# Optimization experiments

Measured on AMD Instinct MI355X. Metric: run time of the kernel, lower is better.

Reference implementation:

```python
import jax, jax.numpy as jnp
import numpy as np

B, T, DIM = 4, 1024, 2048
H, KVH = 16, 4
HD = DIM // H          # 128
G = H // KVH           # GQA group size = 4


def setup_inputs() -> dict:
    key = jax.random.key(0)
    ks = jax.random.split(key, 4)
    s = 1.0 / np.sqrt(DIM)
    x = jax.random.normal(ks[0], (B, T, DIM), jnp.float32)
    Wq = jax.random.normal(ks[1], (DIM, DIM), jnp.float32) * s
    Wkv = jax.random.normal(ks[2], (DIM, 2 * KVH * HD), jnp.float32) * s
    Wo = jax.random.normal(ks[3], (DIM, DIM), jnp.float32) * s
    # RoPE tables (theta=10000, half-split / rotate-half convention)
    inv_freq = 1.0 / (10000.0 ** (np.arange(0, HD, 2, dtype=np.float64) / HD))
    freqs = np.outer(np.arange(T, dtype=np.float64), inv_freq)  # [T, HD/2]
    cos = jnp.asarray(np.cos(freqs), jnp.float32)
    sin = jnp.asarray(np.sin(freqs), jnp.float32)
    return {"x": x, "Wq": Wq, "Wkv": Wkv, "Wo": Wo, "cos": cos, "sin": sin}


def _rope(u, cos, sin):
    # u: [B,T,heads,HD]; cos/sin: [T, HD/2]
    u1, u2 = jnp.split(u, 2, axis=-1)
    c = cos[None, :, None, :]
    s = sin[None, :, None, :]
    return jnp.concatenate([u1 * c - u2 * s, u1 * s + u2 * c], axis=-1)


def reference(x, Wq, Wkv, Wo, cos, sin):
    Bs, Ts, C = x.shape
    q = (x @ Wq).reshape(Bs, Ts, H, HD)
    kv = (x @ Wkv).reshape(Bs, Ts, 2, KVH, HD)
    k, v = kv[:, :, 0], kv[:, :, 1]
    q = _rope(q, cos, sin)
    k = _rope(k, cos, sin)
    # GQA without materializing repeated K/V: fold group dim into q
    qg = q.reshape(Bs, Ts, KVH, G, HD)
    scores = jnp.einsum('bqhgd,bkhd->bhgqk', qg, k) / np.float32(np.sqrt(HD))
    causal = jnp.tril(jnp.ones((Ts, Ts), bool))
    neg = jnp.finfo(scores.dtype).min
    scores = jnp.where(causal, scores, neg)
    att = jax.nn.softmax(scores, axis=-1)
    out = jnp.einsum('bhgqk,bkhd->bqhgd', att, v).reshape(Bs, Ts, C)
    return out @ Wo
```

## Files before the change

kernel.cpp:

```cpp
#include <hip/hip_runtime.h>

typedef unsigned short u16;
typedef unsigned int u32;
typedef __bf16 bf16x8 __attribute__((ext_vector_type(8)));
typedef float f32x4 __attribute__((ext_vector_type(4)));

#define BB   4
#define TT   1024
#define CDIM 2048
#define NH   16
#define NKV  4
#define HDIM 128

__device__ __forceinline__ float b2f(u16 u) {
    union { u32 i; float f; } x; x.i = ((u32)u) << 16; return x.f;
}
__device__ __forceinline__ u16 f2b(float f) {
    union { float f; u32 i; } x; x.f = f;
    u32 r = (x.i + 0x7fffu + ((x.i >> 16) & 1u)) >> 16;
    return (u16)r;
}
__device__ __forceinline__ void async16(const void* g, void* l) {
    __builtin_amdgcn_global_load_lds((const __attribute__((address_space(1))) void*)g,
                                     (__attribute__((address_space(3))) void*)l, 16, 0, 0);
}
template<int N> __device__ __forceinline__ void waitvm() {
    static_assert(N == 0 || N == 3 || N == 4 || N == 6 || N == 7, "unsupported vmcnt");
    if constexpr (N == 0)      asm volatile("s_waitcnt vmcnt(0)" ::: "memory");
    else if constexpr (N == 3) asm volatile("s_waitcnt vmcnt(3)" ::: "memory");
    else if constexpr (N == 4) asm volatile("s_waitcnt vmcnt(4)" ::: "memory");
    else if constexpr (N == 6) asm volatile("s_waitcnt vmcnt(6)" ::: "memory");
    else                       asm volatile("s_waitcnt vmcnt(7)" ::: "memory");
}

__device__ __forceinline__ bool wave_is_f32(const u16* xp) {
    u16 v = xp[(threadIdx.x & 63) * 2];
    int e = (v >> 7) & 0xFF;
    bool bad = (v != 0) && (e < 90 || e > 160);
    return __popcll(__ballot(bad)) > 16;
}

__global__ __launch_bounds__(256) void pre_k(const void* __restrict__ x,
                                             const void* __restrict__ Wq,
                                             const void* __restrict__ Wkv,
                                             const void* __restrict__ Wo,
                                             u16* __restrict__ xb,
                                             u16* __restrict__ csb,
                                             u16* __restrict__ snb,
                                             u16* __restrict__ WqkvT,
                                             u16* __restrict__ WoT,
                                             const void* __restrict__ cs,
                                             const void* __restrict__ sn) {
    const bool f32m = wave_is_f32((const u16*)x);
    int bid = blockIdx.x;
    if (bid < 8320) {
        const void* src; u16* dst; int i;
        if (bid < 8192)      { src = x;  dst = xb;  i = bid * 256 + threadIdx.x; }
        else if (bid < 8256) { src = cs; dst = csb; i = (bid - 8192) * 256 + threadIdx.x; }
        else                 { src = sn; dst = snb; i = (bid - 8256) * 256 + threadIdx.x; }
        union { u16 u[4]; ushort4 v; } o;
        if (f32m) {
            float4 f = ((const float4*)src)[i];
            o.u[0] = f2b(f.x); o.u[1] = f2b(f.y); o.u[2] = f2b(f.z); o.u[3] = f2b(f.w);
        } else {
            o.v = ((const ushort4*)src)[i];
        }
        ((ushort4*)dst)[i] = o.v;
        return;
    }
    __shared__ alignas(16) u16 tile[64 * 65];
    int t = bid - 8320;
    const void* W; u16* WT; int rows, cols, bx, by;
    if (t < 1024)      { W = Wq;  WT = WqkvT;                    rows = 2048; cols = 2048; bx = t & 31;  by = t >> 5; }
    else if (t < 1536) { int l = t - 1024; W = Wkv; WT = WqkvT + (long)2048 * 2048; rows = 2048; cols = 1024; bx = l & 15; by = l >> 4; }
    else               { int l = t - 1536; W = Wo;  WT = WoT;  rows = 2048; cols = 2048; bx = l & 31;   by = l >> 5; }
    const int r0 = by * 64, c0 = bx * 64;
#pragma unroll
    for (int i = 0; i < 16; i++) {
        int c = threadIdx.x + i * 256;
        int rr = c >> 6, cc = c & 63;
        long idx = (long)(r0 + rr) * cols + c0 + cc;
        tile[rr * 65 + cc] = f32m ? f2b(((const float*)W)[idx]) : ((const u16*)W)[idx];
    }
    __syncthreads();
#pragma unroll
    for (int i = 0; i < 16; i++) {
        int c = threadIdx.x + i * 256;
        int rr = c >> 6, cc = c & 63;
        WT[(long)(c0 + rr) * rows + r0 + cc] = tile[cc * 65 + rr];
    }
}

template<int BM, int BN>
__global__ __launch_bounds__(512, 2) void gemm_t(const u16* __restrict__ A,
                                                 const u16* __restrict__ Bt,
                                                 void* __restrict__ C,
                                                 int N, int Kd,
                                                 const u16* __restrict__ xprobe) {
    constexpr int MF  = BM / 32;
    constexpr int NF  = BN / 64;
    constexpr int MF0 = MF / 2, MF1 = MF - MF0;
    constexpr int NF0 = (NF + 1) / 2, NF1 = NF - NF0;
    constexpr int NAU = BM / 64;
    constexpr int NBU = BN / 64;

    __shared__ alignas(16) u16 As[2][BM * 64];
    __shared__ alignas(16) u16 Bs[2][BN * 64];

    const bool f32m = (xprobe != nullptr) && wave_is_f32(xprobe);
    const int tid = threadIdx.x;
    const int w = tid >> 6, lane = tid & 63;
    const int wm = w >> 2, wn = w & 3;
    const int l16 = lane & 15, quad = lane >> 4;
    const long arow0 = (long)blockIdx.y * BM;
    const long brow0 = (long)blockIdx.x * BN;
    const int NT = Kd >> 6;

    const int srow = tid >> 3, scp = tid & 7;
    const long gst = (long)srow * Kd + ((scp ^ (srow & 7)) << 3);
    const int cst = tid << 3;

    const u16* Ab = A + arow0 * Kd;
    const u16* Bb = Bt + brow0 * Kd;

    auto stageA = [&](int buf, int t) {
#pragma unroll
        for (int u = 0; u < NAU; u++)
            async16(Ab + (long)u * 64 * Kd + t * 64 + gst, &As[buf][u * 4096 + cst]);
    };
    auto stageB = [&](int buf, int t) {
#pragma unroll
        for (int u = 0; u < NBU; u++)
            async16(Bb + (long)u * 64 * Kd + t * 64 + gst, &Bs[buf][u * 4096 + cst]);
    };

    const int R0a = wm * (BM / 2) + l16, sA = R0a & 7;
    const int R0b = wn * (BN / 4) + l16, sB = R0b & 7;
    int aoff[2], boff[2];
    aoff[0] = R0a * 64 + ((quad ^ sA) << 3);
    aoff[1] = R0a * 64 + (((4 + quad) ^ sA) << 3);
    boff[0] = R0b * 64 + ((quad ^ sB) << 3);
    boff[1] = R0b * 64 + (((4 + quad) ^ sB) << 3);

    f32x4 acc[MF][NF];
#pragma unroll
    for (int i = 0; i < MF; i++)
#pragma unroll
        for (int j = 0; j < NF; j++) acc[i][j] = {0.f, 0.f, 0.f, 0.f};

    stageB(0, 0); stageA(0, 0); stageB(1, 1); stageA(1, 1);
    waitvm<NAU + NBU>();
    __builtin_amdgcn_s_barrier();

#pragma unroll 1
    for (int t = 0; t < NT; ++t) {
        const int cur = t & 1;
        const u16* pA = &As[cur][0];
        const u16* pB = &Bs[cur][0];
        bf16x8 afLo[MF0][2], afHi[MF1][2], bfA[NF0][2], bfB[NF1][2];

#pragma unroll
        for (int ks = 0; ks < 2; ks++) {
#pragma unroll
            for (int mt = 0; mt < MF0; mt++)
                afLo[mt][ks] = *(const bf16x8*)&pA[aoff[ks] + mt * 1024];
#pragma unroll
            for (int nt = 0; nt < NF0; nt++)
                bfA[nt][ks] = *(const bf16x8*)&pB[boff[ks] + nt * 1024];
#pragma unroll
            for (int nt = 0; nt < NF1; nt++)
                bfB[nt][ks] = *(const bf16x8*)&pB[boff[ks] + (NF0 + nt) * 1024];
        }
        asm volatile("s_waitcnt lgkmcnt(0)" ::: "memory");
        __builtin_amdgcn_sched_barrier(0);
        __builtin_amdgcn_s_setprio(1);
#pragma unroll
        for (int ks = 0; ks < 2; ks++)
#pragma unroll
            for (int mt = 0; mt < MF0; mt++) {
#pragma unroll
                for (int nt = 0; nt < NF0; nt++)
                    acc[mt][nt] = __builtin_amdgcn_mfma_f32_16x16x32_bf16(
                        afLo[mt][ks], bfA[nt][ks], acc[mt][nt], 0, 0, 0);
#pragma unroll
                for (int nt = 0; nt < NF1; nt++)
                    acc[mt][NF0 + nt] = __builtin_amdgcn_mfma_f32_16x16x32_bf16(
                        afLo[mt][ks], bfB[nt][ks], acc[mt][NF0 + nt], 0, 0, 0);
            }
        __builtin_amdgcn_s_setprio(0);

#pragma unroll
        for (int ks = 0; ks < 2; ks++)
#pragma unroll
            for (int mt = 0; mt < MF1; mt++)
                afHi[mt][ks] = *(const bf16x8*)&pA[aoff[ks] + (MF0 + mt) * 1024];
        __builtin_amdgcn_s_barrier();
        if (t + 2 < NT) stageB(cur, t + 2);
        asm volatile("s_waitcnt lgkmcnt(0)" ::: "memory");
        __builtin_amdgcn_sched_barrier(0);
        __builtin_amdgcn_s_setprio(1);
#pragma unroll
        for (int ks = 0; ks < 2; ks++)
#pragma unroll
            for (int mt = 0; mt < MF1; mt++) {
#pragma unroll
                for (int nt = 0; nt < NF1; nt++)
                    acc[MF0 + mt][NF0 + nt] = __builtin_amdgcn_mfma_f32_16x16x32_bf16(
                        afHi[mt][ks], bfB[nt][ks], acc[MF0 + mt][NF0 + nt], 0, 0, 0);
#pragma unroll
                for (int nt = 0; nt < NF0; nt++)
                    acc[MF0 + mt][nt] = __builtin_amdgcn_mfma_f32_16x16x32_bf16(
                        afHi[mt][ks], bfA[nt][ks], acc[MF0 + mt][nt], 0, 0, 0);
            }
        __builtin_amdgcn_s_setprio(0);

        if (t + 1 < NT) {
            if (t + 2 < NT) waitvm<NBU>();
            else            waitvm<0>();
            __builtin_amdgcn_s_barrier();
            if (t + 2 < NT) stageA(cur, t + 2);
        }
    }

#pragma unroll
    for (int mt = 0; mt < MF; mt++) {
#pragma unroll
        for (int nt = 0; nt < NF; nt++) {
            long col = brow0 + wn * (BN / 4) + nt * 16 + l16;
#pragma unroll
            for (int r = 0; r < 4; r++) {
                long row = arow0 + wm * (BM / 2) + mt * 16 + quad * 4 + r;
                if (f32m) ((float*)C)[row * N + col] = acc[mt][nt][r];
                else      ((u16*)C)[row * N + col] = f2b(acc[mt][nt][r]);
            }
        }
    }
}

__global__ __launch_bounds__(256) void prep_k(const u16* __restrict__ QKVraw,
                                              const u16* __restrict__ cs,
                                              const u16* __restrict__ sn,
                                              u16* __restrict__ Qr,
                                              u16* __restrict__ Kr,
                                              u16* __restrict__ Vt) {
    int bid = blockIdx.x;
    if (bid < 16384) {
        int idx = bid * 256 + threadIdx.x;
        int d = idx & 63;
        int t = (idx >> 6) & (TT - 1);
        int bh = idx >> 16;
        long src = ((long)((bh >> 4) * TT + t)) * 3072 + (bh & 15) * HDIM;
        float u1 = b2f(QKVraw[src + d]), u2 = b2f(QKVraw[src + d + 64]);
        float c = b2f(cs[t * 64 + d]), s = b2f(sn[t * 64 + d]);
        long dst = ((long)bh * TT + t) * HDIM;
        Qr[dst + d] = f2b(u1 * c - u2 * s);
        Qr[dst + d + 64] = f2b(u1 * s + u2 * c);
    } else if (bid < 20480) {
        int idx = (bid - 16384) * 256 + threadIdx.x;
        int d = idx & 63;
        int t = (idx >> 6) & (TT - 1);
        int bk = idx >> 16;
        long src = ((long)((bk >> 2) * TT + t)) * 3072 + 2048 + (bk & 3) * HDIM;
        float u1 = b2f(QKVraw[src + d]), u2 = b2f(QKVraw[src + d + 64]);
        float c = b2f(cs[t * 64 + d]), s = b2f(sn[t * 64 + d]);
        long dst = ((long)bk * TT + t) * HDIM;
        Kr[dst + d] = f2b(u1 * c - u2 * s);
        Kr[dst + d + 64] = f2b(u1 * s + u2 * c);
    } else {
        int idx = (bid - 20480) * 256 + threadIdx.x;
        int t = idx & (TT - 1);
        int d = (idx >> 10) & (HDIM - 1);
        int bk = idx >> 17;
        Vt[idx] = QKVraw[((long)(bk >> 2) * TT + t) * 3072 + 2560 + (bk & 3) * HDIM + d];
    }
}

__global__ __launch_bounds__(256) void attn_kernel(const u16* __restrict__ Q,
                                                   const u16* __restrict__ Kr,
                                                   const u16* __restrict__ Vt,
                                                   u16* __restrict__ O) {
    __shared__ alignas(16) u16 Ks[2][64 * 128];
    __shared__ alignas(16) u16 Vts[2][128 * 64];
    __shared__ alignas(16) u16 Ps[64 * 88];

    const int tid = threadIdx.x, w = tid >> 6, lane = tid & 63;
    const int l16 = lane & 15, quad = lane >> 4;
    const float scale2 = 0.08838834764831845f * 1.4426950408889634f;

#pragma unroll 1
    for (int it = 0; it < 2; it++) {
        const int j = it ? (1023 - (int)blockIdx.x) : (int)blockIdx.x;
        const int qt = 15 - (j >> 6);
        const int bh = j & 63;
        const int b = bh >> 4, h = bh & 15;
        const int kvh = h >> 2;
        const long qrow0 = (long)bh * TT + qt * 64;
        const long krow0 = (long)(b * NKV + kvh) * TT;
        const long vbase = ((long)(b * NKV + kvh) * HDIM) * TT;

        __syncthreads();

#pragma unroll
        for (int i = 0; i < 4; i++) {
            int slot0 = (w * 4 + i) * 64;
            int slot = slot0 + lane;
            int row = slot >> 4, cp = slot & 15;
            int cg = (cp & 8) | ((cp ^ row) & 7);
            async16(Q + (qrow0 + row) * HDIM + cg * 8, &Ks[0][slot0 * 8]);
        }
        asm volatile("s_waitcnt vmcnt(0)" ::: "memory");
        bf16x8 qf[4];
        {
            const int Rq = w * 16 + l16;
#pragma unroll
            for (int ds = 0; ds < 4; ds++) {
                int c = ds * 4 + quad;
                qf[ds] = *(const bf16x8*)&Ks[0][Rq * 128 + ((c & 8) | ((c ^ Rq) & 7)) * 8];
            }
        }
        asm volatile("s_waitcnt lgkmcnt(0)" ::: "memory");

#pragma unroll
        for (int i = 0; i < 4; i++) {
            int slot0 = (w * 4 + i) * 64;
            int slot = slot0 + lane;
            int row = slot >> 4, cp = slot & 15;
            int cg = (cp & 8) | ((cp ^ row) & 7);
            async16(Kr + (krow0 + row) * HDIM + cg * 8, &Ks[0][slot0 * 8]);
        }
#pragma unroll
        for (int i = 0; i < 4; i++) {
            int slot0 = (w * 4 + i) * 64;
            int slot = slot0 + lane;
            int row = slot >> 3, cp = slot & 7;
            int cg = cp ^ (row & 7);
            async16(Vt + vbase + (long)row * TT + cg * 8, &Vts[0][slot0 * 8]);
        }
        if (qt >= 1) {
#pragma unroll
            for (int i = 0; i < 4; i++) {
                int slot0 = (w * 4 + i) * 64;
                int slot = slot0 + lane;
                int row = slot >> 4, cp = slot & 15;
                int cg = (cp & 8) | ((cp ^ row) & 7);
                async16(Kr + (krow0 + 64 + row) * HDIM + cg * 8, &Ks[1][slot0 * 8]);
            }
#pragma unroll
            for (int i = 0; i < 4; i++) {
                int slot0 = (w * 4 + i) * 64;
                int slot = slot0 + lane;
                int row = slot >> 3, cp = slot & 7;
                int cg = cp ^ (row & 7);
                async16(Vt + vbase + (long)row * TT + 64 + cg * 8, &Vts[1][slot0 * 8]);
            }
            asm volatile("s_waitcnt vmcnt(8)" ::: "memory");
        } else {
            asm volatile("s_waitcnt vmcnt(0)" ::: "memory");
        }
        asm volatile("s_barrier" ::: "memory");

        f32x4 o[8];
#pragma unroll
        for (int i = 0; i < 8; i++) o[i] = {0.f, 0.f, 0.f, 0.f};
        float m_i = -1.0e30f, l_i = 0.f;
        const int qg = qt * 64 + w * 16 + l16;

#pragma unroll 1
        for (int kt = 0; kt <= qt; kt++) {
            const int cur = kt & 1;
            const u16* ksb = Ks[cur];
            const u16* vsb = Vts[cur];

            f32x4 s[4];
#pragma unroll
            for (int nt = 0; nt < 4; nt++) s[nt] = {0.f, 0.f, 0.f, 0.f};
#pragma unroll
            for (int ds = 0; ds < 4; ds++) {
                int c = ds * 4 + quad;
#pragma unroll
                for (int nt = 0; nt < 4; nt++) {
                    int Rk = nt * 16 + l16;
                    bf16x8 ak = *(const bf16x8*)&ksb[Rk * 128 + ((c & 8) | ((c ^ Rk) & 7)) * 8];
                    s[nt] = __builtin_amdgcn_mfma_f32_16x16x32_bf16(ak, qf[ds], s[nt], 0, 0, 0);
                }
            }

            float p[4][4];
            float mx = -1.0e30f;
            if (kt == qt) {
#pragma unroll
                for (int nt = 0; nt < 4; nt++)
#pragma unroll
                    for (int r = 0; r < 4; r++) {
                        int kcol = kt * 64 + nt * 16 + quad * 4 + r;
                        float v = (kcol <= qg) ? (float)s[nt][r] * scale2 : -1.0e30f;
                        p[nt][r] = v;
                        mx = fmaxf(mx, v);
                    }
            } else {
#pragma unroll
                for (int nt = 0; nt < 4; nt++)
#pragma unroll
                    for (int r = 0; r < 4; r++) {
                        float v = (float)s[nt][r] * scale2;
                        p[nt][r] = v;
                        mx = fmaxf(mx, v);
                    }
            }
            mx = fmaxf(mx, __shfl_xor(mx, 16));
            mx = fmaxf(mx, __shfl_xor(mx, 32));
            float mnew = fmaxf(m_i, mx);
            float alpha = exp2f(m_i - mnew);
            float rs = 0.f;
#pragma unroll
            for (int nt = 0; nt < 4; nt++)
#pragma unroll
                for (int r = 0; r < 4; r++) {
                    float e = exp2f(p[nt][r] - mnew);
                    p[nt][r] = e;
                    rs += e;
                }
            rs += __shfl_xor(rs, 16);
            rs += __shfl_xor(rs, 32);
            l_i = l_i * alpha + rs;

            u32* Psw = (u32*)Ps;
            int pb = (w * 16 + l16) * 44 + quad * 2;
#pragma unroll
            for (int nt = 0; nt < 4; nt++) {
                u32 lo = (u32)f2b(p[nt][0]) | ((u32)f2b(p[nt][1]) << 16);
                u32 hi = (u32)f2b(p[nt][2]) | ((u32)f2b(p[nt][3]) << 16);
                Psw[pb + nt * 8]     = lo;
                Psw[pb + nt * 8 + 1] = hi;
            }
            if (__ballot(mnew != m_i) != 0ULL) {
#pragma unroll
                for (int n8 = 0; n8 < 8; n8++)
#pragma unroll
                    for (int r = 0; r < 4; r++) o[n8][r] *= alpha;
            }
            m_i = mnew;

            asm volatile("s_waitcnt lgkmcnt(0)" ::: "memory");

#pragma unroll
            for (int ks = 0; ks < 2; ks++) {
                bf16x8 bp = *(const bf16x8*)&Ps[(w * 16 + l16) * 88 + ks * 32 + quad * 8];
#pragma unroll
                for (int n8 = 0; n8 < 8; n8++) {
                    int Rv = n8 * 16 + l16;
                    int c = ks * 4 + quad;
                    bf16x8 av = *(const bf16x8*)&vsb[Rv * 64 + (c ^ (Rv & 7)) * 8];
                    o[n8] = __builtin_amdgcn_mfma_f32_16x16x32_bf16(av, bp, o[n8], 0, 0, 0);
                }
            }

            if (kt == qt) break;

            asm volatile("s_waitcnt lgkmcnt(0)" ::: "memory");
            asm volatile("s_barrier" ::: "memory");
            if (kt + 2 <= qt) {
                const int nk = kt + 2;
#pragma unroll
                for (int i = 0; i < 4; i++) {
                    int slot0 = (w * 4 + i) * 64;
                    int slot = slot0 + lane;
                    int row = slot >> 4, cp = slot & 15;
                    int cg = (cp & 8) | ((cp ^ row) & 7);
                    async16(Kr + (krow0 + nk * 64 + row) * HDIM + cg * 8, &Ks[cur][slot0 * 8]);
                }
#pragma unroll
                for (int i = 0; i < 4; i++) {
                    int slot0 = (w * 4 + i) * 64;
                    int slot = slot0 + lane;
                    int row = slot >> 3, cp = slot & 7;
                    int cg = cp ^ (row & 7);
                    async16(Vt + vbase + (long)row * TT + nk * 64 + cg * 8, &Vts[cur][slot0 * 8]);
                }
                asm volatile("s_waitcnt vmcnt(8)" ::: "memory");
            } else {
                asm volatile("s_waitcnt vmcnt(0)" ::: "memory");
            }
            asm volatile("s_barrier" ::: "memory");
        }

        float inv = 1.0f / l_i;
        long obase = ((long)(b * TT + qg)) * CDIM + h * HDIM;
#pragma unroll
        for (int n8 = 0; n8 < 8; n8++) {
            ushort4 st;
            st.x = f2b(o[n8][0] * inv);
            st.y = f2b(o[n8][1] * inv);
            st.z = f2b(o[n8][2] * inv);
            st.w = f2b(o[n8][3] * inv);
            *(ushort4*)&O[obase + n8 * 16 + quad * 4] = st;
        }
    }
}

extern "C" void kernel_launch(void* const* d_in, const int* in_sizes, int n_in,
                              void* d_out, int out_size, void* d_ws, size_t ws_size,
                              hipStream_t stream) {
    const void* x   = d_in[0];
    const void* Wq  = d_in[1];
    const void* Wkv = d_in[2];
    const void* Wo  = d_in[3];
    const void* cs  = d_in[4];
    const void* sn  = d_in[5];

    char* ws = (char*)d_ws;
    const size_t NEED = 105119748;
    if (ws_size < NEED) return;

    u16* WqkvT = (u16*)(ws + 0);
    u16* WoT   = (u16*)(ws + 12582912);
    u16* QKVraw= (u16*)(ws + 20971520);
    u16* Qr    = (u16*)(ws + 46137344);
    u16* Kr    = (u16*)(ws + 62914560);
    u16* Vt    = (u16*)(ws + 67108864);
    u16* ATT   = (u16*)(ws + 71303168);
    u16* xb    = (u16*)(ws + 88080384);
    u16* csb   = (u16*)(ws + 104857600);
    u16* snb   = (u16*)(ws + 104988672);

    pre_k<<<10880, 256, 0, stream>>>(x, Wq, Wkv, Wo, xb, csb, snb, WqkvT, WoT, cs, sn);

    gemm_t<256, 192><<<dim3(16, 16), 512, 0, stream>>>(xb, WqkvT, QKVraw, 3072, 2048, nullptr);

    prep_k<<<28672, 256, 0, stream>>>(QKVraw, csb, snb, Qr, Kr, Vt);

    attn_kernel<<<512, 256, 0, stream>>>(Qr, Kr, Vt, ATT);

    gemm_t<128, 256><<<dim3(8, 32), 512, 0, stream>>>(ATT, WoT, d_out, 2048, 2048, (const u16*)x);
}
```

Before: 302.5 us.

## Split GEMM mainloop into four MFMA phases with interleaved half-tile async staging

Restructures the double-buffered bf16 GEMM mainloop into four compute phases, each preceded by LDS fragment loads, a barrier and an async global-to-LDS stage of half of the next tile's A or B rows. The prologue now preloads only half of the next B tile, and the rest of the next-tile loads are spread across the iteration. The goal is to interleave memory traffic with MFMA work more finely and shorten the exposed wait per iteration. In exchange it adds more barriers per iteration and a full vmcnt(0) wait, which could add stalls.

```diff
diff --git a/kernel.cpp b/kernel.cpp
--- a/kernel.cpp
+++ b/kernel.cpp
@@ -25,12 +25,16 @@
                                      (__attribute__((address_space(3))) void*)l, 16, 0, 0);
 }
 template<int N> __device__ __forceinline__ void waitvm() {
-    static_assert(N == 0 || N == 3 || N == 4 || N == 6 || N == 7, "unsupported vmcnt");
+    static_assert(N >= 0 && N <= 8, "unsupported vmcnt");
     if constexpr (N == 0)      asm volatile("s_waitcnt vmcnt(0)" ::: "memory");
+    else if constexpr (N == 1) asm volatile("s_waitcnt vmcnt(1)" ::: "memory");
+    else if constexpr (N == 2) asm volatile("s_waitcnt vmcnt(2)" ::: "memory");
     else if constexpr (N == 3) asm volatile("s_waitcnt vmcnt(3)" ::: "memory");
     else if constexpr (N == 4) asm volatile("s_waitcnt vmcnt(4)" ::: "memory");
+    else if constexpr (N == 5) asm volatile("s_waitcnt vmcnt(5)" ::: "memory");
     else if constexpr (N == 6) asm volatile("s_waitcnt vmcnt(6)" ::: "memory");
-    else                       asm volatile("s_waitcnt vmcnt(7)" ::: "memory");
+    else if constexpr (N == 7) asm volatile("s_waitcnt vmcnt(7)" ::: "memory");
+    else                       asm volatile("s_waitcnt vmcnt(8)" ::: "memory");
 }
 
 __device__ __forceinline__ bool wave_is_f32(const u16* xp) {
@@ -103,6 +107,8 @@
     constexpr int NF0 = (NF + 1) / 2, NF1 = NF - NF0;
     constexpr int NAU = BM / 64;
     constexpr int NBU = BN / 64;
+    constexpr int NAL = NAU / 2;
+    constexpr int NBL = NBU / 2;
 
     __shared__ alignas(16) u16 As[2][BM * 64];
     __shared__ alignas(16) u16 Bs[2][BN * 64];
@@ -123,15 +129,17 @@
     const u16* Ab = A + arow0 * Kd;
     const u16* Bb = Bt + brow0 * Kd;
 
-    auto stageA = [&](int buf, int t) {
+    auto stageA = [&](int buf, int t, int u0, int u1) {
 #pragma unroll
         for (int u = 0; u < NAU; u++)
-            async16(Ab + (long)u * 64 * Kd + t * 64 + gst, &As[buf][u * 4096 + cst]);
+            if (u >= u0 && u < u1)
+                async16(Ab + (long)u * 64 * Kd + t * 64 + gst, &As[buf][u * 4096 + cst]);
     };
-    auto stageB = [&](int buf, int t) {
+    auto stageB = [&](int buf, int t, int u0, int u1) {
 #pragma unroll
         for (int u = 0; u < NBU; u++)
-            async16(Bb + (long)u * 64 * Kd + t * 64 + gst, &Bs[buf][u * 4096 + cst]);
+            if (u >= u0 && u < u1)
+                async16(Bb + (long)u * 64 * Kd + t * 64 + gst, &Bs[buf][u * 4096 + cst]);
     };
 
     const int R0a = wm * (BM / 2) + l16, sA = R0a & 7;
@@ -148,13 +156,15 @@
 #pragma unroll
         for (int j = 0; j < NF; j++) acc[i][j] = {0.f, 0.f, 0.f, 0.f};
 
-    stageB(0, 0); stageA(0, 0); stageB(1, 1); stageA(1, 1);
-    waitvm<NAU + NBU>();
+    stageB(0, 0, 0, NBU);
+    stageA(0, 0, 0, NAU);
+    stageB(1, 1, 0, NBL);
+    waitvm<NBL>();
     __builtin_amdgcn_s_barrier();
 
 #pragma unroll 1
     for (int t = 0; t < NT; ++t) {
-        const int cur = t & 1;
+        const int cur = t & 1, nxt = cur ^ 1;
         const u16* pA = &As[cur][0];
         const u16* pB = &Bs[cur][0];
         bf16x8 afLo[MF0][2], afHi[MF1][2], bfA[NF0][2], bfB[NF1][2];
@@ -167,26 +177,40 @@
 #pragma unroll
             for (int nt = 0; nt < NF0; nt++)
                 bfA[nt][ks] = *(const bf16x8*)&pB[boff[ks] + nt * 1024];
-#pragma unroll
-            for (int nt = 0; nt < NF1; nt++)
-                bfB[nt][ks] = *(const bf16x8*)&pB[boff[ks] + (NF0 + nt) * 1024];
-        }
+        }
+        if (t + 1 < NT) stageB(nxt, t + 1, NBL, NBU);
+        __builtin_amdgcn_s_barrier();
         asm volatile("s_waitcnt lgkmcnt(0)" ::: "memory");
         __builtin_amdgcn_sched_barrier(0);
         __builtin_amdgcn_s_setprio(1);
 #pragma unroll
         for (int ks = 0; ks < 2; ks++)
 #pragma unroll
-            for (int mt = 0; mt < MF0; mt++) {
+            for (int mt = 0; mt < MF0; mt++)
 #pragma unroll
                 for (int nt = 0; nt < NF0; nt++)
                     acc[mt][nt] = __builtin_amdgcn_mfma_f32_16x16x32_bf16(
                         afLo[mt][ks], bfA[nt][ks], acc[mt][nt], 0, 0, 0);
+        __builtin_amdgcn_s_setprio(0);
+
+#pragma unroll
+        for (int ks = 0; ks < 2; ks++)
+#pragma unroll
+            for (int nt = 0; nt < NF1; nt++)
+                bfB[nt][ks] = *(const bf16x8*)&pB[boff[ks] + (NF0 + nt) * 1024];
+        if (t + 1 < NT) stageA(nxt, t + 1, 0, NAL);
+        __builtin_amdgcn_s_barrier();
+        asm volatile("s_waitcnt lgkmcnt(0)" ::: "memory");
+        __builtin_amdgcn_sched_barrier(0);
+        __builtin_amdgcn_s_setprio(1);
+#pragma unroll
+        for (int ks = 0; ks < 2; ks++)
+#pragma unroll
+            for (int mt = 0; mt < MF0; mt++)
 #pragma unroll
                 for (int nt = 0; nt < NF1; nt++)
                     acc[mt][NF0 + nt] = __builtin_amdgcn_mfma_f32_16x16x32_bf16(
                         afLo[mt][ks], bfB[nt][ks], acc[mt][NF0 + nt], 0, 0, 0);
-            }
         __builtin_amdgcn_s_setprio(0);
 
 #pragma unroll
@@ -194,32 +218,37 @@
 #pragma unroll
             for (int mt = 0; mt < MF1; mt++)
                 afHi[mt][ks] = *(const bf16x8*)&pA[aoff[ks] + (MF0 + mt) * 1024];
+        if (t + 1 < NT) stageA(nxt, t + 1, NAL, NAU);
         __builtin_amdgcn_s_barrier();
-        if (t + 2 < NT) stageB(cur, t + 2);
         asm volatile("s_waitcnt lgkmcnt(0)" ::: "memory");
         __builtin_amdgcn_sched_barrier(0);
         __builtin_amdgcn_s_setprio(1);
 #pragma unroll
         for (int ks = 0; ks < 2; ks++)
 #pragma unroll
-            for (int mt = 0; mt < MF1; mt++) {
+            for (int mt = 0; mt < MF1; mt++)
 #pragma unroll
                 for (int nt = 0; nt < NF1; nt++)
                     acc[MF0 + mt][NF0 + nt] = __builtin_amdgcn_mfma_f32_16x16x32_bf16(
                         afHi[mt][ks], bfB[nt][ks], acc[MF0 + mt][NF0 + nt], 0, 0, 0);
+        __builtin_amdgcn_s_setprio(0);
+
+        if (t + 1 < NT) {
+            asm volatile("s_waitcnt vmcnt(0)" ::: "memory");
+            __builtin_amdgcn_s_barrier();
+            if (t + 2 < NT) stageB(cur, t + 2, 0, NBL);
+        }
+        __builtin_amdgcn_sched_barrier(0);
+        __builtin_amdgcn_s_setprio(1);
+#pragma unroll
+        for (int ks = 0; ks < 2; ks++)
+#pragma unroll
+            for (int mt = 0; mt < MF1; mt++)
 #pragma unroll
                 for (int nt = 0; nt < NF0; nt++)
                     acc[MF0 + mt][nt] = __builtin_amdgcn_mfma_f32_16x16x32_bf16(
                         afHi[mt][ks], bfA[nt][ks], acc[MF0 + mt][nt], 0, 0, 0);
-            }
         __builtin_amdgcn_s_setprio(0);
-
-        if (t + 1 < NT) {
-            if (t + 2 < NT) waitvm<NBU>();
-            else            waitvm<0>();
-            __builtin_amdgcn_s_barrier();
-            if (t + 2 < NT) stageA(cur, t + 2);
-        }
     }
 
 #pragma unroll
```

Result: slower. 315.6 us (+4.3%).
